# Kernel optimization log

Hardware: AMD Instinct MI355X
Metric: run time of the kernel (lower is better)

The kernel has to match this reference:

```python
import jax, jax.numpy as jnp
import numpy as np

WBITS = 4
ZERO = 2.0 ** (WBITS - 1)  # symmetric zero-point = 8


def _dequant(q, s):
    # q: [in, out] int codes in [0, 2^wbits); s: [in//group, out] group scales
    g = q.shape[0] // s.shape[0]
    scale_full = jnp.repeat(s, g, axis=0)          # [in, out]
    return (q.astype(s.dtype) - ZERO) * scale_full


def setup_inputs() -> dict:
    key = jax.random.key(0)
    ks = jax.random.split(key, 7)
    H, I = 4096, 11008
    G = 128
    x = jax.random.normal(ks[0], (4, 2048, H), dtype=jnp.float32)
    gate_q = jax.random.randint(ks[1], (H, I), 0, 2 ** WBITS, dtype=jnp.int32)
    up_q = jax.random.randint(ks[2], (H, I), 0, 2 ** WBITS, dtype=jnp.int32)
    down_q = jax.random.randint(ks[3], (I, H), 0, 2 ** WBITS, dtype=jnp.int32)
    # small positive scales, typical of 4-bit quantized weights
    gate_s = jax.random.uniform(ks[4], (H // G, I), dtype=jnp.float32) * 0.01
    up_s = jax.random.uniform(ks[5], (H // G, I), dtype=jnp.float32) * 0.01
    down_s = jax.random.uniform(ks[6], (I // G, H), dtype=jnp.float32) * 0.01
    return {"x": x, "gate_q": gate_q, "gate_s": gate_s, "up_q": up_q,
            "up_s": up_s, "down_q": down_q, "down_s": down_s}


def reference(x, gate_q, gate_s, up_q, up_s, down_q, down_s):
    # LlamaMLP.forward: down_proj(act_fn(gate_proj(x)) * up_proj(x))
    Wg = _dequant(gate_q, gate_s)   # [H, I]
    Wu = _dequant(up_q, up_s)       # [H, I]
    Wd = _dequant(down_q, down_s)   # [I, H]
    g = jnp.einsum('bsh,hi->bsi', x, Wg)
    u = jnp.einsum('bsh,hi->bsi', x, Wu)
    return jnp.einsum('bsi,ih->bsh', jax.nn.silu(g) * u, Wd)
```

## Files before the change

kernel.cpp:

```cpp
#include <hip/hip_runtime.h>
#include <hip/hip_bf16.h>
#include <cstdint>
#include <cstddef>

typedef __bf16 bf16_t;
typedef __bf16 bf16x8 __attribute__((ext_vector_type(8)));
typedef float f32x4 __attribute__((ext_vector_type(4)));
typedef unsigned int u32;
typedef u32 u32x4 __attribute__((ext_vector_type(4)));

#define H_DIM 4096
#define I_DIM 11008

__device__ __forceinline__ u32 pack_bf16(float a, float b) {
    union { __bf16 h[2]; u32 u; } r;
    r.h[0] = (__bf16)a;
    r.h[1] = (__bf16)b;
    return r.u;
}

__device__ __forceinline__ void gload16(const bf16_t* g, char* l) {
    __builtin_amdgcn_global_load_lds(
        (const __attribute__((address_space(1))) u32*)g,
        (__attribute__((address_space(3))) u32*)l, 16, 0, 0);
}

#define ASM_VMCNT6 asm volatile("s_waitcnt vmcnt(6)" ::: "memory")
#define ASM_VMCNT3 asm volatile("s_waitcnt vmcnt(3)" ::: "memory")
#define ASM_VMCNT0 asm volatile("s_waitcnt vmcnt(0)" ::: "memory")
#define ASM_LGKM0  asm volatile("s_waitcnt lgkmcnt(0)" ::: "memory")
#define ASM_BAR    asm volatile("s_barrier" ::: "memory")

__global__ __launch_bounds__(256) void k_dequant_pack(const int* __restrict__ Q,
                                                      const float* __restrict__ S,
                                                      bf16_t* __restrict__ W,
                                                      int K, int N) {
    __shared__ bf16_t tile[128][40];
    const int tid = threadIdx.x;
    const int k0 = blockIdx.x * 32, n0 = blockIdx.y * 128;
    const int grp = k0 >> 7;
    const int c4 = (tid & 31) * 4;
    const int kr = tid >> 5;
    float4 sc = *(const float4*)(S + (size_t)grp * N + n0 + c4);
#pragma unroll
    for (int p = 0; p < 4; ++p) {
        const int k = kr + p * 8;
        int4 q = *(const int4*)(Q + (size_t)(k0 + k) * N + n0 + c4);
        tile[c4 + 0][k] = (bf16_t)fmaf((float)q.x, sc.x, -8.f * sc.x);
        tile[c4 + 1][k] = (bf16_t)fmaf((float)q.y, sc.y, -8.f * sc.y);
        tile[c4 + 2][k] = (bf16_t)fmaf((float)q.z, sc.z, -8.f * sc.z);
        tile[c4 + 3][k] = (bf16_t)fmaf((float)q.w, sc.w, -8.f * sc.w);
    }
    __syncthreads();
    bf16_t* blk = W + (((size_t)blockIdx.y * (K / 32) + blockIdx.x) << 12);
#pragma unroll
    for (int j = 0; j < 2; ++j) {
        const int u = j * 256 + tid;
        const int cg = u >> 6, ln = u & 63;
        u32x4 v = *(const u32x4*)((const char*)tile +
                                  (size_t)(cg * 16 + (ln & 15)) * 80 + (ln >> 4) * 16);
        *(u32x4*)(blk + (cg << 9) + (ln << 3)) = v;
    }
}

template <int KDIM>
__global__ __launch_bounds__(512, 2) void k_gateup(const float* __restrict__ x,
                                                   const bf16_t* __restrict__ Wg,
                                                   const bf16_t* __restrict__ Wu,
                                                   bf16_t* __restrict__ hp, int Nb) {
    constexpr int NT = KDIM / 32;
    __shared__ char smem[131072];

    const int tid = threadIdx.x, lane = tid & 63, wid = tid >> 6;
    const int wr = wid >> 1, wc = wid & 1;
    const int m0 = blockIdx.x * 256, n0 = blockIdx.y * 128;

    f32x4 accg[4][4], accu[4][4];
#pragma unroll
    for (int i = 0; i < 4; ++i)
#pragma unroll
        for (int j = 0; j < 4; ++j) { accg[i][j] = (f32x4)0.f; accu[i][j] = (f32x4)0.f; }

    const int arow = tid >> 1, ahalf = tid & 1;
    const float* xsrc = x + (size_t)(m0 + arow) * KDIM + ahalf * 16;
    const u32 wa0 = (u32)(((arow >> 4) << 10) | (((ahalf * 2) * 16 + (arow & 15)) << 4));
    const u32 wa1 = wa0 + 256;

    const bf16_t* wgB = Wg + (((size_t)(n0 >> 7) * NT) << 12);
    const bf16_t* wuB = Wu + (((size_t)(n0 >> 7) * NT) << 12);
    const u32 bsegG = (u32)((wid << 9) + (lane << 3));
    const u32 bsegL = (u32)(wid << 10);

    f32x4 preA[4], preB[4];

    auto issueB = [&](int kt) {
        char* b0 = smem + 65536 + ((kt & 3) << 13) + bsegL;
        char* b1 = smem + 98304 + ((kt & 3) << 13) + bsegL;
        gload16(wgB + (((size_t)kt) << 12) + bsegG, b0);
        gload16(wuB + (((size_t)kt) << 12) + bsegG, b1);
    };
    auto issueF = [&](int kt, f32x4 (&pre)[4]) {
        const float* s = xsrc + (size_t)kt * 32;
#pragma unroll
        for (int i = 0; i < 4; ++i) pre[i] = *(const f32x4*)(s + i * 4);
    };
    auto dswriteA = [&](int t1, f32x4 (&pre)[4]) {
        u32x4 w0, w1;
        w0.x = pack_bf16(pre[0].x, pre[0].y); w0.y = pack_bf16(pre[0].z, pre[0].w);
        w0.z = pack_bf16(pre[1].x, pre[1].y); w0.w = pack_bf16(pre[1].z, pre[1].w);
        w1.x = pack_bf16(pre[2].x, pre[2].y); w1.y = pack_bf16(pre[2].z, pre[2].w);
        w1.z = pack_bf16(pre[3].x, pre[3].y); w1.w = pack_bf16(pre[3].z, pre[3].w);
        char* ab = smem + ((t1 & 3) << 14);
        *(u32x4*)(ab + wa0) = w0;
        *(u32x4*)(ab + wa1) = w1;
    };

    auto tile_body = [&](int t, f32x4 (&pre)[4]) {
        const char* abuf = smem + ((t & 3) << 14);
        const char* b0buf = smem + 65536 + ((t & 3) << 13);
        const char* b1buf = smem + 98304 + ((t & 3) << 13);
        const u32 fo = (u32)(lane << 4);
        bf16x8 fa[4], f0[4], f1[4];
#pragma unroll
        for (int f = 0; f < 4; ++f) {
            fa[f] = *(const bf16x8*)(abuf + (((wr * 4 + f) << 10) + fo));
            f0[f] = *(const bf16x8*)(b0buf + (((wc * 4 + f) << 10) + fo));
            f1[f] = *(const bf16x8*)(b1buf + (((wc * 4 + f) << 10) + fo));
        }
        if (t <= NT - 3) { ASM_VMCNT6; } else { ASM_VMCNT0; }
        if (t + 1 < NT) dswriteA(t + 1, pre);
        if (t + 3 < NT) { issueB(t + 3); issueF(t + 3, pre); }
        ASM_LGKM0;
        __builtin_amdgcn_s_setprio(1);
#pragma unroll
        for (int fn = 0; fn < 4; ++fn)
#pragma unroll
            for (int fm = 0; fm < 4; ++fm) {
                accg[fm][fn] = __builtin_amdgcn_mfma_f32_16x16x32_bf16(fa[fm], f0[fn], accg[fm][fn], 0, 0, 0);
                accu[fm][fn] = __builtin_amdgcn_mfma_f32_16x16x32_bf16(fa[fm], f1[fn], accu[fm][fn], 0, 0, 0);
            }
        __builtin_amdgcn_s_setprio(0);
        ASM_BAR;
    };

    issueB(0); issueF(0, preA);
    issueB(1); issueF(1, preB);
    ASM_VMCNT6;
    dswriteA(0, preA);
    issueB(2); issueF(2, preA);
    ASM_LGKM0;
    ASM_BAR;

    for (int t = 0; t < NT; t += 2) {
        tile_body(t, preB);
        tile_body(t + 1, preA);
    }

    bf16_t* bounce = (bf16_t*)smem;
    const int ehr = lane >> 4, col16 = lane & 15;
#pragma unroll
    for (int fm = 0; fm < 4; ++fm)
#pragma unroll
        for (int fn = 0; fn < 4; ++fn)
#pragma unroll
            for (int r = 0; r < 4; ++r) {
                float g = accg[fm][fn][r];
                float u = accu[fm][fn][r];
                float h = (g / (1.f + __expf(-g))) * u;
                const int row_l = wr * 64 + fm * 16 + ehr * 4 + r;
                const int col_l = wc * 64 + fn * 16 + col16;
                bounce[row_l * 136 + col_l] = (bf16_t)h;
            }
    ASM_LGKM0;
    ASM_BAR;
    const size_t hblk = (size_t)blockIdx.x * (Nb / 32) + (n0 >> 5);
#pragma unroll
    for (int j = 0; j < 8; ++j) {
        const int u = j * 512 + tid;
        const int ktl = u >> 10, rg = (u >> 6) & 15, ln = u & 63;
        u32x4 v = *(const u32x4*)((const char*)bounce +
                                  (size_t)(rg * 16 + (ln & 15)) * 272 + ktl * 64 + (ln >> 4) * 16);
        *(u32x4*)(hp + ((hblk + ktl) << 13) + (rg << 9) + (ln << 3)) = v;
    }
}

template <int KDIM>
__global__ __launch_bounds__(512, 2) void k_down(const bf16_t* __restrict__ hp,
                                                 const bf16_t* __restrict__ Wd,
                                                 float* __restrict__ out, int Nb) {
    constexpr int NT = KDIM / 32;
    __shared__ char smem[98304];

    const int tid = threadIdx.x, lane = tid & 63, wid = tid >> 6;
    const int wr = wid >> 1, wc = wid & 1;
    const int m0 = blockIdx.x * 256, n0 = blockIdx.y * 128;

    f32x4 acc[4][4];
#pragma unroll
    for (int i = 0; i < 4; ++i)
#pragma unroll
        for (int j = 0; j < 4; ++j) acc[i][j] = (f32x4)0.f;

    const bf16_t* hpB = hp + (((size_t)blockIdx.x * NT) << 13);
    const bf16_t* wdB = Wd + (((size_t)(n0 >> 7) * NT) << 12);
    const u32 lseg = (u32)(lane << 3);

    auto issue = [&](int kt) {
        char* ab = smem + ((kt & 3) << 14);
        char* bb = smem + 65536 + ((kt & 3) << 13);
        const bf16_t* as = hpB + (((size_t)kt) << 13);
        const bf16_t* bs = wdB + (((size_t)kt) << 12);
        gload16(as + ((wid * 2 + 0) << 9) + lseg, ab + ((wid * 2 + 0) << 10));
        gload16(as + ((wid * 2 + 1) << 9) + lseg, ab + ((wid * 2 + 1) << 10));
        gload16(bs + (wid << 9) + lseg, bb + (wid << 10));
    };

    issue(0); issue(1); issue(2);
    ASM_VMCNT6;
    ASM_BAR;

    for (int t = 0; t < NT; ++t) {
        const char* abuf = smem + ((t & 3) << 14);
        const char* bbuf = smem + 65536 + ((t & 3) << 13);
        const u32 fo = (u32)(lane << 4);
        bf16x8 fa[4], fb[4];
#pragma unroll
        for (int f = 0; f < 4; ++f) {
            fa[f] = *(const bf16x8*)(abuf + (((wr * 4 + f) << 10) + fo));
            fb[f] = *(const bf16x8*)(bbuf + (((wc * 4 + f) << 10) + fo));
        }
        if (t <= NT - 3) { ASM_VMCNT3; } else { ASM_VMCNT0; }
        if (t + 3 < NT) issue(t + 3);
        ASM_LGKM0;
        __builtin_amdgcn_s_setprio(1);
#pragma unroll
        for (int fn = 0; fn < 4; ++fn)
#pragma unroll
            for (int fm = 0; fm < 4; ++fm)
                acc[fm][fn] = __builtin_amdgcn_mfma_f32_16x16x32_bf16(fa[fm], fb[fn], acc[fm][fn], 0, 0, 0);
        __builtin_amdgcn_s_setprio(0);
        ASM_BAR;
    }

    const int ehr = lane >> 4, col16 = lane & 15;
#pragma unroll
    for (int fm = 0; fm < 4; ++fm)
#pragma unroll
        for (int fn = 0; fn < 4; ++fn) {
            const int col = n0 + wc * 64 + fn * 16 + col16;
#pragma unroll
            for (int r = 0; r < 4; ++r) {
                const int row = m0 + wr * 64 + fm * 16 + ehr * 4 + r;
                out[(size_t)row * Nb + col] = acc[fm][fn][r];
            }
        }
}

extern "C" void kernel_launch(void* const* d_in, const int* in_sizes, int n_in,
                              void* d_out, int out_size, void* d_ws, size_t ws_size,
                              hipStream_t stream) {
    const float* x      = (const float*)d_in[0];
    const int*   gate_q = (const int*)d_in[1];
    const float* gate_s = (const float*)d_in[2];
    const int*   up_q   = (const int*)d_in[3];
    const float* up_s   = (const float*)d_in[4];
    const int*   down_q = (const int*)d_in[5];
    const float* down_s = (const float*)d_in[6];
    float*       out    = (float*)d_out;

    const int  H = H_DIM, I = I_DIM;
    const long M = (long)in_sizes[0] / H;

    char*        ws = (char*)d_ws;
    const size_t wb = (size_t)H * I * sizeof(bf16_t);
    bf16_t* wg = (bf16_t*)ws;
    bf16_t* wu = (bf16_t*)(ws + wb);
    bf16_t* wd = (bf16_t*)(ws + 2 * wb);
    bf16_t* hp = (bf16_t*)(ws + 3 * wb);

    long avail = (long)ws_size - (long)(3 * wb);
    long C = avail > 0 ? avail / ((long)I * (long)sizeof(bf16_t)) : 256;
    C = (C / 256) * 256;
    if (C > M) C = M;
    if (C < 256) C = 256;

    dim3 dq1(H / 32, I / 128);
    k_dequant_pack<<<dq1, 256, 0, stream>>>(gate_q, gate_s, wg, H, I);
    k_dequant_pack<<<dq1, 256, 0, stream>>>(up_q, up_s, wu, H, I);
    dim3 dq2(I / 32, H / 128);
    k_dequant_pack<<<dq2, 256, 0, stream>>>(down_q, down_s, wd, I, H);

    for (long c0 = 0; c0 < M; c0 += C) {
        const long mc = (M - c0 < C) ? (M - c0) : C;
        dim3 g1((unsigned)(mc / 256), (unsigned)(I / 128));
        k_gateup<H_DIM><<<g1, 512, 0, stream>>>(x + (size_t)c0 * H, wg, wu, hp, I);
        dim3 g2((unsigned)(mc / 256), (unsigned)(H / 128));
        k_down<I_DIM><<<g2, 512, 0, stream>>>(hp, wd, out + (size_t)c0 * H, H);
    }
}
```

Measured before the change: 2.675 ms.

## Pre-pack activations to bf16 and double-buffer LDS fragment reads in GEMMs

Adds a kernel that converts x from fp32 to bf16 once and stores it in the tiled MFMA layout, so the gate/up GEMM can fetch A tiles with direct global-to-LDS loads instead of per-tile fp32 register loads, packing and LDS writes. Both GEMM main loops are restructured to read the next tile's fragments from LDS into a second register set while the current tile's MFMAs run, with a scheduling fence and the next global prefetch issued after compute. This lowers per-iteration latency and removes redundant fp32 traffic across the many N-tiles. In exchange it uses more workspace and more VGPRs, which may hurt occupancy or cause spills.

```diff
diff --git a/kernel.cpp b/kernel.cpp
--- a/kernel.cpp
+++ b/kernel.cpp
@@ -25,11 +25,12 @@
         (__attribute__((address_space(3))) u32*)l, 16, 0, 0);
 }
 
-#define ASM_VMCNT6 asm volatile("s_waitcnt vmcnt(6)" ::: "memory")
+#define ASM_VMCNT4 asm volatile("s_waitcnt vmcnt(4)" ::: "memory")
 #define ASM_VMCNT3 asm volatile("s_waitcnt vmcnt(3)" ::: "memory")
 #define ASM_VMCNT0 asm volatile("s_waitcnt vmcnt(0)" ::: "memory")
 #define ASM_LGKM0  asm volatile("s_waitcnt lgkmcnt(0)" ::: "memory")
 #define ASM_BAR    asm volatile("s_barrier" ::: "memory")
+#define SCHED_FENCE __builtin_amdgcn_sched_barrier(0)
 
 __global__ __launch_bounds__(256) void k_dequant_pack(const int* __restrict__ Q,
                                                       const float* __restrict__ S,
@@ -63,8 +64,35 @@
     }
 }
 
+__global__ __launch_bounds__(256) void k_cvt_pack(const float* __restrict__ x,
+                                                  bf16_t* __restrict__ xp, int K) {
+    __shared__ bf16_t tile[256][40];
+    const int tid = threadIdx.x;
+    const int m0 = blockIdx.x * 256, k0 = blockIdx.y * 32;
+    const int rr = tid >> 3, kq = (tid & 7) * 4;
+#pragma unroll
+    for (int p = 0; p < 8; ++p) {
+        const int row = rr + p * 32;
+        float4 v = *(const float4*)(x + (size_t)(m0 + row) * K + k0 + kq);
+        uint2 o;
+        o.x = pack_bf16(v.x, v.y);
+        o.y = pack_bf16(v.z, v.w);
+        *(uint2*)&tile[row][kq] = o;
+    }
+    __syncthreads();
+    bf16_t* blk = xp + (((size_t)blockIdx.x * (K / 32) + blockIdx.y) << 13);
+#pragma unroll
+    for (int j = 0; j < 4; ++j) {
+        const int u = j * 256 + tid;
+        const int un = u >> 6, ln = u & 63;
+        u32x4 v = *(const u32x4*)((const char*)tile +
+                                  (size_t)(un * 16 + (ln & 15)) * 80 + (ln >> 4) * 16);
+        *(u32x4*)(blk + (un << 9) + (ln << 3)) = v;
+    }
+}
+
 template <int KDIM>
-__global__ __launch_bounds__(512, 2) void k_gateup(const float* __restrict__ x,
+__global__ __launch_bounds__(512, 2) void k_gateup(const bf16_t* __restrict__ xp,
                                                    const bf16_t* __restrict__ Wg,
                                                    const bf16_t* __restrict__ Wu,
                                                    bf16_t* __restrict__ hp, int Nb) {
@@ -73,7 +101,8 @@
 
     const int tid = threadIdx.x, lane = tid & 63, wid = tid >> 6;
     const int wr = wid >> 1, wc = wid & 1;
-    const int m0 = blockIdx.x * 256, n0 = blockIdx.y * 128;
+    const int mt = blockIdx.x, ntile = blockIdx.y;
+    const int n0 = ntile * 128;
 
     f32x4 accg[4][4], accu[4][4];
 #pragma unroll
@@ -81,79 +110,64 @@
 #pragma unroll
         for (int j = 0; j < 4; ++j) { accg[i][j] = (f32x4)0.f; accu[i][j] = (f32x4)0.f; }
 
-    const int arow = tid >> 1, ahalf = tid & 1;
-    const float* xsrc = x + (size_t)(m0 + arow) * KDIM + ahalf * 16;
-    const u32 wa0 = (u32)(((arow >> 4) << 10) | (((ahalf * 2) * 16 + (arow & 15)) << 4));
-    const u32 wa1 = wa0 + 256;
-
-    const bf16_t* wgB = Wg + (((size_t)(n0 >> 7) * NT) << 12);
-    const bf16_t* wuB = Wu + (((size_t)(n0 >> 7) * NT) << 12);
-    const u32 bsegG = (u32)((wid << 9) + (lane << 3));
-    const u32 bsegL = (u32)(wid << 10);
-
-    f32x4 preA[4], preB[4];
-
-    auto issueB = [&](int kt) {
-        char* b0 = smem + 65536 + ((kt & 3) << 13) + bsegL;
-        char* b1 = smem + 98304 + ((kt & 3) << 13) + bsegL;
-        gload16(wgB + (((size_t)kt) << 12) + bsegG, b0);
-        gload16(wuB + (((size_t)kt) << 12) + bsegG, b1);
-    };
-    auto issueF = [&](int kt, f32x4 (&pre)[4]) {
-        const float* s = xsrc + (size_t)kt * 32;
-#pragma unroll
-        for (int i = 0; i < 4; ++i) pre[i] = *(const f32x4*)(s + i * 4);
-    };
-    auto dswriteA = [&](int t1, f32x4 (&pre)[4]) {
-        u32x4 w0, w1;
-        w0.x = pack_bf16(pre[0].x, pre[0].y); w0.y = pack_bf16(pre[0].z, pre[0].w);
-        w0.z = pack_bf16(pre[1].x, pre[1].y); w0.w = pack_bf16(pre[1].z, pre[1].w);
-        w1.x = pack_bf16(pre[2].x, pre[2].y); w1.y = pack_bf16(pre[2].z, pre[2].w);
-        w1.z = pack_bf16(pre[3].x, pre[3].y); w1.w = pack_bf16(pre[3].z, pre[3].w);
-        char* ab = smem + ((t1 & 3) << 14);
-        *(u32x4*)(ab + wa0) = w0;
-        *(u32x4*)(ab + wa1) = w1;
-    };
-
-    auto tile_body = [&](int t, f32x4 (&pre)[4]) {
-        const char* abuf = smem + ((t & 3) << 14);
-        const char* b0buf = smem + 65536 + ((t & 3) << 13);
-        const char* b1buf = smem + 98304 + ((t & 3) << 13);
+    const bf16_t* xA  = xp + (((size_t)mt * NT) << 13);
+    const bf16_t* wgB = Wg + (((size_t)ntile * NT) << 12);
+    const bf16_t* wuB = Wu + (((size_t)ntile * NT) << 12);
+    const u32 bseg = (u32)((wid << 9) + (lane << 3));
+    const u32 lseg = (u32)(lane << 3);
+
+    auto issue = [&](int kt) {
+        char* ab = smem + ((kt & 3) << 14);
+        char* b0 = smem + 65536 + ((kt & 3) << 13);
+        char* b1 = smem + 98304 + ((kt & 3) << 13);
+        const bf16_t* as = xA + (((size_t)kt) << 13);
+        gload16(as + ((wid * 2 + 0) << 9) + lseg, ab + ((wid * 2 + 0) << 10));
+        gload16(as + ((wid * 2 + 1) << 9) + lseg, ab + ((wid * 2 + 1) << 10));
+        gload16(wgB + (((size_t)kt) << 12) + bseg, b0 + (wid << 10));
+        gload16(wuB + (((size_t)kt) << 12) + bseg, b1 + (wid << 10));
+    };
+    auto readf = [&](int kt, bf16x8 (&fr)[12]) {
+        const char* ab = smem + ((kt & 3) << 14);
+        const char* b0 = smem + 65536 + ((kt & 3) << 13);
+        const char* b1 = smem + 98304 + ((kt & 3) << 13);
         const u32 fo = (u32)(lane << 4);
-        bf16x8 fa[4], f0[4], f1[4];
 #pragma unroll
         for (int f = 0; f < 4; ++f) {
-            fa[f] = *(const bf16x8*)(abuf + (((wr * 4 + f) << 10) + fo));
-            f0[f] = *(const bf16x8*)(b0buf + (((wc * 4 + f) << 10) + fo));
-            f1[f] = *(const bf16x8*)(b1buf + (((wc * 4 + f) << 10) + fo));
-        }
-        if (t <= NT - 3) { ASM_VMCNT6; } else { ASM_VMCNT0; }
-        if (t + 1 < NT) dswriteA(t + 1, pre);
-        if (t + 3 < NT) { issueB(t + 3); issueF(t + 3, pre); }
-        ASM_LGKM0;
+            fr[f]     = *(const bf16x8*)(ab + (((wr * 4 + f) << 10) + fo));
+            fr[4 + f] = *(const bf16x8*)(b0 + (((wc * 4 + f) << 10) + fo));
+            fr[8 + f] = *(const bf16x8*)(b1 + (((wc * 4 + f) << 10) + fo));
+        }
+    };
+    auto body = [&](int t, bf16x8 (&cur)[12], bf16x8 (&nxt)[12]) {
+        if (t + 1 < NT) readf(t + 1, nxt);
+        SCHED_FENCE;
         __builtin_amdgcn_s_setprio(1);
 #pragma unroll
         for (int fn = 0; fn < 4; ++fn)
 #pragma unroll
             for (int fm = 0; fm < 4; ++fm) {
-                accg[fm][fn] = __builtin_amdgcn_mfma_f32_16x16x32_bf16(fa[fm], f0[fn], accg[fm][fn], 0, 0, 0);
-                accu[fm][fn] = __builtin_amdgcn_mfma_f32_16x16x32_bf16(fa[fm], f1[fn], accu[fm][fn], 0, 0, 0);
+                accg[fm][fn] = __builtin_amdgcn_mfma_f32_16x16x32_bf16(cur[fm], cur[4 + fn], accg[fm][fn], 0, 0, 0);
+                accu[fm][fn] = __builtin_amdgcn_mfma_f32_16x16x32_bf16(cur[fm], cur[8 + fn], accu[fm][fn], 0, 0, 0);
             }
         __builtin_amdgcn_s_setprio(0);
+        if (t + 3 < NT) {
+            issue(t + 3);
+            ASM_VMCNT4;
+        } else {
+            ASM_VMCNT0;
+        }
         ASM_BAR;
     };
 
-    issueB(0); issueF(0, preA);
-    issueB(1); issueF(1, preB);
-    ASM_VMCNT6;
-    dswriteA(0, preA);
-    issueB(2); issueF(2, preA);
-    ASM_LGKM0;
+    bf16x8 fA[12], fB[12];
+    issue(0); issue(1); issue(2);
+    ASM_VMCNT4;
     ASM_BAR;
+    readf(0, fA);
 
     for (int t = 0; t < NT; t += 2) {
-        tile_body(t, preB);
-        tile_body(t + 1, preA);
+        body(t, fA, fB);
+        body(t + 1, fB, fA);
     }
 
     bf16_t* bounce = (bf16_t*)smem;
@@ -173,7 +187,7 @@
             }
     ASM_LGKM0;
     ASM_BAR;
-    const size_t hblk = (size_t)blockIdx.x * (Nb / 32) + (n0 >> 5);
+    const size_t hblk = (size_t)mt * (Nb / 32) + (n0 >> 5);
 #pragma unroll
     for (int j = 0; j < 8; ++j) {
         const int u = j * 512 + tid;
@@ -193,7 +207,8 @@
 
     const int tid = threadIdx.x, lane = tid & 63, wid = tid >> 6;
     const int wr = wid >> 1, wc = wid & 1;
-    const int m0 = blockIdx.x * 256, n0 = blockIdx.y * 128;
+    const int mt = blockIdx.x, ntile = blockIdx.y;
+    const int m0 = mt * 256, n0 = ntile * 128;
 
     f32x4 acc[4][4];
 #pragma unroll
@@ -201,8 +216,8 @@
 #pragma unroll
         for (int j = 0; j < 4; ++j) acc[i][j] = (f32x4)0.f;
 
-    const bf16_t* hpB = hp + (((size_t)blockIdx.x * NT) << 13);
-    const bf16_t* wdB = Wd + (((size_t)(n0 >> 7) * NT) << 12);
+    const bf16_t* hpB = hp + (((size_t)mt * NT) << 13);
+    const bf16_t* wdB = Wd + (((size_t)ntile * NT) << 12);
     const u32 lseg = (u32)(lane << 3);
 
     auto issue = [&](int kt) {
@@ -214,32 +229,44 @@
         gload16(as + ((wid * 2 + 1) << 9) + lseg, ab + ((wid * 2 + 1) << 10));
         gload16(bs + (wid << 9) + lseg, bb + (wid << 10));
     };
-
+    auto readf = [&](int kt, bf16x8 (&fr)[8]) {
+        const char* ab = smem + ((kt & 3) << 14);
+        const char* bb = smem + 65536 + ((kt & 3) << 13);
+        const u32 fo = (u32)(lane << 4);
+#pragma unroll
+        for (int f = 0; f < 4; ++f) {
+            fr[f]     = *(const bf16x8*)(ab + (((wr * 4 + f) << 10) + fo));
+            fr[4 + f] = *(const bf16x8*)(bb + (((wc * 4 + f) << 10) + fo));
+        }
+    };
+    auto body = [&](int t, bf16x8 (&cur)[8], bf16x8 (&nxt)[8]) {
+        if (t + 1 < NT) readf(t + 1, nxt);
+        SCHED_FENCE;
+        __builtin_amdgcn_s_setprio(1);
+#pragma unroll
+        for (int fn = 0; fn < 4; ++fn)
+#pragma unroll
+            for (int fm = 0; fm < 4; ++fm)
+                acc[fm][fn] = __builtin_amdgcn_mfma_f32_16x16x32_bf16(cur[fm], cur[4 + fn], acc[fm][fn], 0, 0, 0);
+        __builtin_amdgcn_s_setprio(0);
+        if (t + 3 < NT) {
+            issue(t + 3);
+            ASM_VMCNT3;
+        } else {
+            ASM_VMCNT0;
+        }
+        ASM_BAR;
+    };
+
+    bf16x8 fA[8], fB[8];
     issue(0); issue(1); issue(2);
-    ASM_VMCNT6;
+    ASM_VMCNT3;
     ASM_BAR;
-
-    for (int t = 0; t < NT; ++t) {
-        const char* abuf = smem + ((t & 3) << 14);
-        const char* bbuf = smem + 65536 + ((t & 3) << 13);
-        const u32 fo = (u32)(lane << 4);
-        bf16x8 fa[4], fb[4];
-#pragma unroll
-        for (int f = 0; f < 4; ++f) {
-            fa[f] = *(const bf16x8*)(abuf + (((wr * 4 + f) << 10) + fo));
-            fb[f] = *(const bf16x8*)(bbuf + (((wc * 4 + f) << 10) + fo));
-        }
-        if (t <= NT - 3) { ASM_VMCNT3; } else { ASM_VMCNT0; }
-        if (t + 3 < NT) issue(t + 3);
-        ASM_LGKM0;
-        __builtin_amdgcn_s_setprio(1);
-#pragma unroll
-        for (int fn = 0; fn < 4; ++fn)
-#pragma unroll
-            for (int fm = 0; fm < 4; ++fm)
-                acc[fm][fn] = __builtin_amdgcn_mfma_f32_16x16x32_bf16(fa[fm], fb[fn], acc[fm][fn], 0, 0, 0);
-        __builtin_amdgcn_s_setprio(0);
-        ASM_BAR;
+    readf(0, fA);
+
+    for (int t = 0; t < NT; t += 2) {
+        body(t, fA, fB);
+        body(t + 1, fB, fA);
     }
 
     const int ehr = lane >> 4, col16 = lane & 15;
@@ -272,13 +299,15 @@
     const long M = (long)in_sizes[0] / H;
 
     char*        ws = (char*)d_ws;
-    const size_t wb = (size_t)H * I * sizeof(bf16_t);
+    const size_t wb  = (size_t)H * I * sizeof(bf16_t);
+    const size_t xpb = (size_t)M * H * sizeof(bf16_t);
     bf16_t* wg = (bf16_t*)ws;
     bf16_t* wu = (bf16_t*)(ws + wb);
     bf16_t* wd = (bf16_t*)(ws + 2 * wb);
-    bf16_t* hp = (bf16_t*)(ws + 3 * wb);
-
-    long avail = (long)ws_size - (long)(3 * wb);
+    bf16_t* xpk = (bf16_t*)(ws + 3 * wb);
+    bf16_t* hp  = (bf16_t*)(ws + 3 * wb + xpb);
+
+    long avail = (long)ws_size - (long)(3 * wb + xpb);
     long C = avail > 0 ? avail / ((long)I * (long)sizeof(bf16_t)) : 256;
     C = (C / 256) * 256;
     if (C > M) C = M;
@@ -289,11 +318,14 @@
     k_dequant_pack<<<dq1, 256, 0, stream>>>(up_q, up_s, wu, H, I);
     dim3 dq2(I / 32, H / 128);
     k_dequant_pack<<<dq2, 256, 0, stream>>>(down_q, down_s, wd, I, H);
+    dim3 dcv((unsigned)(M / 256), H / 32);
+    k_cvt_pack<<<dcv, 256, 0, stream>>>(x, xpk, H);
 
     for (long c0 = 0; c0 < M; c0 += C) {
         const long mc = (M - c0 < C) ? (M - c0) : C;
         dim3 g1((unsigned)(mc / 256), (unsigned)(I / 128));
-        k_gateup<H_DIM><<<g1, 512, 0, stream>>>(x + (size_t)c0 * H, wg, wu, hp, I);
+        k_gateup<H_DIM><<<g1, 512, 0, stream>>>(xpk + (size_t)(c0 / 256) * ((size_t)H_DIM / 32 << 13),
+                                                wg, wu, hp, I);
         dim3 g2((unsigned)(mc / 256), (unsigned)(H / 128));
         k_down<I_DIM><<<g2, 512, 0, stream>>>(hp, wd, out + (size_t)c0 * H, H);
     }
```

Result: faster. 2.410 ms (-9.9%).
